# Kernel tuning notes

Measured on AMD Instinct MI355X. Metric: run time of the kernel, lower is better.

## Reference

```python
import jax, jax.numpy as jnp
import numpy as np

B, T, C, H, W, NC = 128, 32, 512, 8, 32, 6625
HH = C // 2  # per-direction LSTM hidden


def setup_inputs() -> dict:
    key = jax.random.key(0)
    ks = jax.random.split(key, 20)
    u = lambda k, shape, n: jax.random.uniform(k, shape, jnp.float32, -1.0 / np.sqrt(n), 1.0 / np.sqrt(n))
    return dict(
        feature=jax.random.normal(ks[0], (B, C, H, W), jnp.float32),
        attention_map=jax.random.uniform(ks[1], (B, T, H, W), jnp.float32) + 1e-3,
        text=jax.random.randint(ks[2], (B, T), 0, NC),
        text_length=jnp.full((B,), T, dtype=jnp.int32),
        char_embeddings=jax.random.normal(ks[3], (NC, C), jnp.float32),
        lstm_w_ih_f=u(ks[4], (4 * HH, C), HH),
        lstm_w_hh_f=u(ks[5], (4 * HH, HH), HH),
        lstm_b_ih_f=u(ks[6], (4 * HH,), HH),
        lstm_b_hh_f=u(ks[7], (4 * HH,), HH),
        lstm_w_ih_b=u(ks[8], (4 * HH, C), HH),
        lstm_w_hh_b=u(ks[9], (4 * HH, HH), HH),
        lstm_b_ih_b=u(ks[10], (4 * HH,), HH),
        lstm_b_hh_b=u(ks[11], (4 * HH,), HH),
        gru_w_ih=u(ks[12], (3 * C, 2 * C), C),
        gru_w_hh=u(ks[13], (3 * C, C), C),
        gru_b_ih=u(ks[14], (3 * C,), C),
        gru_b_hh=u(ks[15], (3 * C,), C),
        gen_w=u(ks[16], (NC, C), C),
        gen_b=u(ks[17], (NC,), C),
    )


def _lstm_dir(xs, w_ih, w_hh, b_ih, b_hh):
    # xs: [T, B, C] -> hs: [T, B, HH]; PyTorch gate order i, f, g, o
    b = xs.shape[1]
    hh = w_hh.shape[1]
    def step(carry, xt):
        h, c = carry
        g = xt @ w_ih.T + h @ w_hh.T + (b_ih + b_hh)
        i, f, gg, o = jnp.split(g, 4, axis=-1)
        c = jax.nn.sigmoid(f) * c + jax.nn.sigmoid(i) * jnp.tanh(gg)
        h = jax.nn.sigmoid(o) * jnp.tanh(c)
        return (h, c), h
    h0 = jnp.zeros((b, hh), xs.dtype)
    _, hs = jax.lax.scan(step, (h0, h0), xs)
    return hs


def reference(feature, attention_map, text, text_length, char_embeddings,
              lstm_w_ih_f, lstm_w_hh_f, lstm_b_ih_f, lstm_b_hh_f,
              lstm_w_ih_b, lstm_w_hh_b, lstm_b_ih_b, lstm_b_hh_b,
              gru_w_ih, gru_w_hh, gru_b_ih, gru_b_hh, gen_w, gen_b):
    b, c, h, w = feature.shape
    t = attention_map.shape[1]
    # normalize attention over spatial dims, attention-pool features: [T, B, C]
    att = attention_map / attention_map.sum(axis=(2, 3), keepdims=True)
    cseq = jnp.einsum('bchw,bthw->tbc', feature, att)
    # bidirectional LSTM (dropout is identity in eval mode)
    hs_f = _lstm_dir(cseq, lstm_w_ih_f, lstm_w_hh_f, lstm_b_ih_f, lstm_b_hh_f)
    hs_b = _lstm_dir(cseq[::-1], lstm_w_ih_b, lstm_w_hh_b, lstm_b_ih_b, lstm_b_hh_b)[::-1]
    cseq = jnp.concatenate([hs_f, hs_b], axis=-1)  # [T, B, C]
    # teacher-forced previous-char embeddings: step 0 uses index 0
    prev_idx = jnp.concatenate([jnp.zeros((b, 1), text.dtype), text[:, :-1]], axis=1)  # [B, T]
    prev_emb = jnp.transpose(char_embeddings[prev_idx], (1, 0, 2))  # [T, B, C]
    # GRUCell decode; PyTorch gate order r, z, n
    def gru_step(hid, inp):
        ct, pe = inp
        x = jnp.concatenate([ct, pe], axis=-1)  # [B, 2C]
        gi = x @ gru_w_ih.T + gru_b_ih
        gh = hid @ gru_w_hh.T + gru_b_hh
        ir, iz, inn = jnp.split(gi, 3, axis=-1)
        hr, hz, hn = jnp.split(gh, 3, axis=-1)
        r = jax.nn.sigmoid(ir + hr)
        z = jax.nn.sigmoid(iz + hz)
        n = jnp.tanh(inn + r * hn)
        hid = (1.0 - z) * n + z * hid
        return hid, hid
    h0 = jnp.zeros((b, c), cseq.dtype)
    _, gru_res = jax.lax.scan(gru_step, h0, (cseq, prev_emb))  # [T, B, C]
    logits = gru_res @ gen_w.T + gen_b  # [T, B, NC]
    # pack per text_length; lengths are all == T so this equals a reshape
    out_res = jnp.transpose(logits, (1, 0, 2)).reshape(b * t, -1)
    out_attentions = att.reshape(b * t, h, w)
    return (out_res, out_attentions)
```

## Files before the change

kernel.cpp:

```cpp
#include <hip/hip_runtime.h>
#include <math.h>

typedef __attribute__((ext_vector_type(8))) short sh8;
typedef __attribute__((ext_vector_type(4))) short sh4;
typedef __attribute__((ext_vector_type(4))) float f4;

__device__ inline short f2bf(float f) {
    union { float f; unsigned u; } v; v.f = f;
    unsigned u = v.u;
    return (short)((u + 0x7fffu + ((u >> 16) & 1u)) >> 16);
}
__device__ inline float sigm(float x) { return 1.f / (1.f + expf(-x)); }

__device__ inline sh8 frag8(const float* __restrict__ p) {
    f4 a = *(const f4*)p;
    f4 b = *(const f4*)(p + 4);
    sh8 r;
    r[0]=f2bf(a[0]); r[1]=f2bf(a[1]); r[2]=f2bf(a[2]); r[3]=f2bf(a[3]);
    r[4]=f2bf(b[0]); r[5]=f2bf(b[1]); r[6]=f2bf(b[2]); r[7]=f2bf(b[3]);
    return r;
}

__device__ inline sh8 cload_b128(const short* p) {
    sh8 r;
    asm volatile("global_load_dwordx4 %0, %1, off sc0 sc1" : "=v"(r) : "v"(p));
    return r;
}

__device__ inline void grp_signal(int* myflag, int epoch) {
    asm volatile("s_waitcnt vmcnt(0)" ::: "memory");
    __syncthreads();
    if (threadIdx.x == 0)
        __hip_atomic_store(myflag, epoch, __ATOMIC_RELAXED, __HIP_MEMORY_SCOPE_AGENT);
}
__device__ inline void grp_wait(const int* fbase, int nb, int epoch) {
    if (threadIdx.x < 64) {
        int lane = threadIdx.x;
        bool need = lane < nb;
        const int* fp = fbase + lane * 16;
        while (true) {
            int v = need ? __hip_atomic_load(fp, __ATOMIC_RELAXED, __HIP_MEMORY_SCOPE_AGENT)
                         : 0x7fffffff;
            if (__ballot(need && (v < epoch)) == 0ull) break;
            __builtin_amdgcn_s_sleep(1);
        }
    }
    __syncthreads();
}

__global__ void zero_ctr(int* c, int n) {
    int i = blockIdx.x * blockDim.x + threadIdx.x;
    if (i < n) c[i] = 0;
}

struct CvtPack { const float* s[7]; short* d[7]; int n4[7]; };
__global__ void cvt_bf16(CvtPack p) {
    int job = blockIdx.y;
    const f4* s = (const f4*)p.s[job];
    sh4* d = (sh4*)p.d[job];
    int n4 = p.n4[job];
    for (int i = blockIdx.x * blockDim.x + threadIdx.x; i < n4; i += gridDim.x * blockDim.x) {
        f4 v = s[i];
        sh4 o; o[0]=f2bf(v[0]); o[1]=f2bf(v[1]); o[2]=f2bf(v[2]); o[3]=f2bf(v[3]);
        d[i] = o;
    }
}

__global__ void bias_prep(const float* bihf, const float* bhhf,
                          const float* bihb, const float* bhhb, float* biasL) {
    int n = blockIdx.x * blockDim.x + threadIdx.x;
    biasL[n] = (n < 1024) ? bihf[n] + bhhf[n] : bihb[n - 1024] + bhhb[n - 1024];
}

__global__ void att_norm(const float* __restrict__ att, float* __restrict__ outA) {
    int row = blockIdx.x;
    int tid = threadIdx.x;
    const float* p = att + (size_t)row * 256;
    f4 v = *(const f4*)(p + tid * 4);
    float sum = v[0] + v[1] + v[2] + v[3];
    #pragma unroll
    for (int off = 32; off; off >>= 1) sum += __shfl_down(sum, off);
    float inv = 1.f / __shfl(sum, 0);
    f4 o; o[0]=v[0]*inv; o[1]=v[1]*inv; o[2]=v[2]*inv; o[3]=v[3]*inv;
    *(f4*)(outA + (size_t)row * 256 + tid * 4) = o;
}

__global__ __launch_bounds__(256)
void pool_gemm(const float* __restrict__ feature, const float* __restrict__ att,
               short* __restrict__ cseqb) {
    int bz = blockIdx.y;
    const float* A  = feature + (size_t)bz * 512 * 256;
    const float* Wt = att + (size_t)bz * 32 * 256;
    int wave = threadIdx.x >> 6, lane = threadIdx.x & 63, r = lane & 15, hh = lane >> 4;
    int m0 = blockIdx.x * 64 + wave * 16;
    f4 acc[2] = {};
    const float* ar = A  + (size_t)(m0 + r) * 256 + hh * 8;
    const float* w0 = Wt + (size_t)r * 256 + hh * 8;
    const float* w1 = Wt + (size_t)(16 + r) * 256 + hh * 8;
    for (int kk = 0; kk < 256; kk += 32) {
        sh8 af = frag8(ar + kk);
        acc[0] = __builtin_amdgcn_mfma_f32_16x16x32_bf16(af, frag8(w0 + kk), acc[0], 0, 0, 0);
        acc[1] = __builtin_amdgcn_mfma_f32_16x16x32_bf16(af, frag8(w1 + kk), acc[1], 0, 0, 0);
    }
    #pragma unroll
    for (int j = 0; j < 2; j++) {
        int t = j * 16 + r;
        #pragma unroll
        for (int reg = 0; reg < 4; reg++) {
            int c = m0 + hh * 4 + reg;
            cseqb[(size_t)t * 65536 + (size_t)bz * 512 + c] = f2bf(acc[j][reg]);
        }
    }
}

template<int MODE>
__global__ __launch_bounds__(256)
void gemm128(const short* __restrict__ A, const short* __restrict__ W,
             const float* __restrict__ bias1, const float* __restrict__ bias2,
             float* __restrict__ out, int M, int N, int K) {
    __shared__ short lds[2][2][4096];
    const int tid = threadIdx.x, wave = tid >> 6, lane = tid & 63;
    const int r = lane & 15, hh = lane >> 4;
    const int wm = wave >> 1, wn = wave & 1;
    const int m0 = blockIdx.x * 128, n0 = blockIdx.y * 128;

    const int c0 = tid, c1 = 256 + tid;
    const int r0 = c0 >> 2, r1 = c1 >> 2;
    const int s0 = ((c0 & 3) ^ ((r0 >> 1) & 3));
    const int s1 = ((c1 & 3) ^ ((r1 >> 1) & 3));
    const short* gA0 = A + (size_t)(m0 + r0) * K + s0 * 8;
    const short* gA1 = A + (size_t)(m0 + r1) * K + s1 * 8;
    int wr0 = n0 + r0; if (wr0 > N - 1) wr0 = N - 1;
    int wr1 = n0 + r1; if (wr1 > N - 1) wr1 = N - 1;
    const short* gW0 = W + (size_t)wr0 * K + s0 * 8;
    const short* gW1 = W + (size_t)wr1 * K + s1 * 8;
    const int lo0 = (wave * 64) * 8, lo1 = (256 + wave * 64) * 8;

    auto stage = [&](int buf, int kt) {
        int ko = kt * 32;
        __builtin_amdgcn_global_load_lds((const __attribute__((address_space(1))) void*)(gA0 + ko),
            (__attribute__((address_space(3))) void*)&lds[buf][0][lo0], 16, 0, 0);
        __builtin_amdgcn_global_load_lds((const __attribute__((address_space(1))) void*)(gA1 + ko),
            (__attribute__((address_space(3))) void*)&lds[buf][0][lo1], 16, 0, 0);
        __builtin_amdgcn_global_load_lds((const __attribute__((address_space(1))) void*)(gW0 + ko),
            (__attribute__((address_space(3))) void*)&lds[buf][1][lo0], 16, 0, 0);
        __builtin_amdgcn_global_load_lds((const __attribute__((address_space(1))) void*)(gW1 + ko),
            (__attribute__((address_space(3))) void*)&lds[buf][1][lo1], 16, 0, 0);
    };

    f4 acc[4][4] = {};
    const int NT = K / 32;
    int cur = 0;

    stage(0, 0);
    __syncthreads();
    for (int kt = 0; kt < NT; ++kt) {
        if (kt + 1 < NT) stage(cur ^ 1, kt + 1);
        const char* As = (const char*)&lds[cur][0][0];
        const char* Ws = (const char*)&lds[cur][1][0];
        sh8 a[4], b[4];
        #pragma unroll
        for (int i = 0; i < 4; i++) {
            int row = wm * 64 + i * 16 + r;
            a[i] = *(const sh8*)(As + row * 64 + ((hh ^ ((row >> 1) & 3)) * 16));
        }
        #pragma unroll
        for (int i = 0; i < 4; i++) {
            int row = wn * 64 + i * 16 + r;
            b[i] = *(const sh8*)(Ws + row * 64 + ((hh ^ ((row >> 1) & 3)) * 16));
        }
        #pragma unroll
        for (int i = 0; i < 4; i++)
            #pragma unroll
            for (int j = 0; j < 4; j++)
                acc[i][j] = __builtin_amdgcn_mfma_f32_16x16x32_bf16(a[i], b[j], acc[i][j], 0, 0, 0);
        __syncthreads();
        cur ^= 1;
    }

    #pragma unroll
    for (int j = 0; j < 4; j++) {
        int n = n0 + wn * 64 + j * 16 + r;
        if (n >= N) continue;
        float bs = (bias1 ? bias1[n] : 0.f) + (bias2 ? bias2[n] : 0.f);
        #pragma unroll
        for (int i = 0; i < 4; i++) {
            #pragma unroll
            for (int reg = 0; reg < 4; reg++) {
                int m = m0 + wm * 64 + i * 16 + hh * 4 + reg;
                size_t idx;
                if (MODE == 0) idx = (size_t)m * N + n;
                else           idx = ((size_t)(m & 127) * 32 + (m >> 7)) * (size_t)N + n;
                out[idx] = acc[i][j][reg] + bs;
            }
        }
    }
}

__global__ void emb_fill(const int* __restrict__ text, const float* __restrict__ emb,
                         short* __restrict__ xcatb) {
    int n = blockIdx.x;
    int t = n >> 7, b = n & 127;
    int idx = (t == 0) ? 0 : text[b * 32 + (t - 1)];
    const f4* src = (const f4*)(emb + (size_t)idx * 512);
    sh4* dst = (sh4*)(xcatb + (size_t)n * 1024 + 512);
    for (int j = threadIdx.x; j < 128; j += 64) {
        f4 v = src[j];
        sh4 o; o[0]=f2bf(v[0]); o[1]=f2bf(v[1]); o[2]=f2bf(v[2]); o[3]=f2bf(v[3]);
        dst[j] = o;
    }
}

__global__ __launch_bounds__(128)
void lstm_chain(const float* __restrict__ xfb,
                const short* __restrict__ whhf_b, const short* __restrict__ whhb_b,
                short* __restrict__ xcatb,
                int* __restrict__ flags) {
    __shared__ short wlds[64 * 256];
    const int blk = blockIdx.x;
    const int dir = blk >> 6;
    const int mg  = (blk >> 4) & 3;
    const int ug  = blk & 15;
    const int m0 = mg * 32, u0 = ug * 16;
    const short* whh = dir ? whhb_b : whhf_b;
    const int dcol = dir ? 256 : 0;

    int* grp_flags = flags + (dir * 4 + mg) * 16 * 16;
    int* my_flag   = grp_flags + ug * 16;

    const int tid = threadIdx.x, mt = tid >> 6, lane = tid & 63;
    const int r = lane & 15, hh = lane >> 4;
    unsigned* xcat32 = (unsigned*)xcatb;

    for (int i = 0; i < 16; i++) {
        int c = i * 128 + tid;
        int col = c >> 5, off = c & 31;
        int g = col >> 4, ul = col & 15;
        sh8 v = *(const sh8*)(whh + ((size_t)(g * 256 + u0 + ul)) * 256 + off * 8);
        *(sh8*)((char*)wlds + col * 512 + ((off * 16) ^ ((col & 7) << 4))) = v;
    }
    __syncthreads();

    const int arow_m = m0 + mt * 16 + r;
    const int u = u0 + r;
    const int mb = m0 + mt * 16 + hh * 4;
    float c_state[4] = {0.f, 0.f, 0.f, 0.f};

    float xv[4][4];
    {
        const int t0 = dir ? 31 : 0;
        #pragma unroll
        for (int g = 0; g < 4; g++)
            #pragma unroll
            for (int reg = 0; reg < 4; reg++)
                xv[g][reg] = xfb[((size_t)t0 * 128 + mb + reg) * 2048 + dir * 1024 + g * 256 + u];
    }

    for (int s = 0; s < 32; s++) {
        const int t = dir ? (31 - s) : s;
        f4 acc[4] = {};
        if (s > 0) {
            grp_wait(grp_flags, 16, s);
            const int tp = dir ? (t + 1) : (t - 1);
            const short* arow = xcatb + ((size_t)tp * 128 + arow_m) * 1024 + dcol + hh * 8;
            sh8 afr[8];
            #pragma unroll
            for (int kk = 0; kk < 8; kk++) afr[kk] = cload_b128(arow + kk * 32);
            asm volatile("s_waitcnt vmcnt(0)" ::: "memory");
            __builtin_amdgcn_sched_barrier(0);
            #pragma unroll
            for (int kk = 0; kk < 8; kk++) {
                #pragma unroll
                for (int g = 0; g < 4; g++) {
                    int colr = g * 16 + r;
                    sh8 bf = *(const sh8*)((const char*)wlds + colr * 512 +
                              (((kk * 64 + hh * 16)) ^ ((colr & 7) << 4)));
                    acc[g] = __builtin_amdgcn_mfma_f32_16x16x32_bf16(afr[kk], bf, acc[g], 0, 0, 0);
                }
            }
        }
        #pragma unroll
        for (int reg = 0; reg < 4; reg++) {
            int m = mb + reg;
            float gI = acc[0][reg] + xv[0][reg];
            float gF = acc[1][reg] + xv[1][reg];
            float gG = acc[2][reg] + xv[2][reg];
            float gO = acc[3][reg] + xv[3][reg];
            float cn = sigm(gF) * c_state[reg] + sigm(gI) * tanhf(gG);
            c_state[reg] = cn;
            float h = sigm(gO) * tanhf(cn);
            unsigned hb = (unsigned)(unsigned short)f2bf(h);
            unsigned pb = (unsigned)__shfl_xor((int)hb, 1, 64);
            if (!(r & 1))
                __hip_atomic_store(&xcat32[((size_t)t * 128 + m) * 512 + ((dcol + u) >> 1)],
                                   hb | (pb << 16), __ATOMIC_RELAXED, __HIP_MEMORY_SCOPE_AGENT);
        }
        if (s < 31) {
            grp_signal(my_flag, s + 1);
            const int tn = dir ? (t - 1) : (t + 1);
            #pragma unroll
            for (int g = 0; g < 4; g++)
                #pragma unroll
                for (int reg = 0; reg < 4; reg++)
                    xv[g][reg] = xfb[((size_t)tn * 128 + mb + reg) * 2048 + dir * 1024 + g * 256 + u];
        }
    }
}

__global__ __launch_bounds__(128)
void gru_chain(const float* __restrict__ gi,
               const short* __restrict__ gwhh_b, const float* __restrict__ bhh,
               short* __restrict__ gresb,
               int* __restrict__ flags) {
    __shared__ short wlds[48 * 512];
    const int blk = blockIdx.x;
    const int mg = blk >> 5, ug = blk & 31;
    const int m0 = mg * 32, u0 = ug * 16;

    int* grp_flags = flags + mg * 32 * 16;
    int* my_flag   = grp_flags + ug * 16;

    const int tid = threadIdx.x, mt = tid >> 6, lane = tid & 63;
    const int r = lane & 15, hh = lane >> 4;
    unsigned* gres32 = (unsigned*)gresb;

    for (int i = 0; i < 24; i++) {
        int c = i * 128 + tid;
        int col = c >> 6, off = c & 63;
        int g = col >> 4, ul = col & 15;
        sh8 v = *(const sh8*)(gwhh_b + ((size_t)(g * 512 + u0 + ul)) * 512 + off * 8);
        *(sh8*)((char*)wlds + col * 1024 + ((off * 16) ^ ((col & 7) << 4))) = v;
    }
    __syncthreads();

    const int arow_m = m0 + mt * 16 + r;
    const int u = u0 + r;
    const int mb = m0 + mt * 16 + hh * 4;
    const float bh_r = bhh[u], bh_z = bhh[512 + u], bh_n = bhh[1024 + u];
    float h_state[4] = {0.f, 0.f, 0.f, 0.f};

    float gv[3][4];
    #pragma unroll
    for (int g = 0; g < 3; g++)
        #pragma unroll
        for (int reg = 0; reg < 4; reg++)
            gv[g][reg] = gi[((size_t)(mb + reg)) * 1536 + g * 512 + u];

    for (int t = 0; t < 32; t++) {
        f4 acc[3] = {};
        if (t > 0) {
            grp_wait(grp_flags, 32, t);
            const short* arow = gresb + ((size_t)(t - 1) * 128 + arow_m) * 512 + hh * 8;
            sh8 afr[16];
            #pragma unroll
            for (int kk = 0; kk < 16; kk++) afr[kk] = cload_b128(arow + kk * 32);
            asm volatile("s_waitcnt vmcnt(0)" ::: "memory");
            __builtin_amdgcn_sched_barrier(0);
            #pragma unroll
            for (int kk = 0; kk < 16; kk++) {
                #pragma unroll
                for (int g = 0; g < 3; g++) {
                    int colr = g * 16 + r;
                    sh8 bf = *(const sh8*)((const char*)wlds + colr * 1024 +
                              (((kk * 64 + hh * 16)) ^ ((colr & 7) << 4)));
                    acc[g] = __builtin_amdgcn_mfma_f32_16x16x32_bf16(afr[kk], bf, acc[g], 0, 0, 0);
                }
            }
        }
        #pragma unroll
        for (int reg = 0; reg < 4; reg++) {
            int m = mb + reg;
            float rr = sigm(gv[0][reg] + acc[0][reg] + bh_r);
            float zz = sigm(gv[1][reg] + acc[1][reg] + bh_z);
            float nn = tanhf(gv[2][reg] + rr * (acc[2][reg] + bh_n));
            float h = (1.f - zz) * nn + zz * h_state[reg];
            h_state[reg] = h;
            unsigned hb = (unsigned)(unsigned short)f2bf(h);
            unsigned pb = (unsigned)__shfl_xor((int)hb, 1, 64);
            if (!(r & 1))
                __hip_atomic_store(&gres32[((size_t)t * 128 + m) * 256 + (u >> 1)],
                                   hb | (pb << 16), __ATOMIC_RELAXED, __HIP_MEMORY_SCOPE_AGENT);
        }
        if (t < 31) {
            grp_signal(my_flag, t + 1);
            #pragma unroll
            for (int g = 0; g < 3; g++)
                #pragma unroll
                for (int reg = 0; reg < 4; reg++)
                    gv[g][reg] = gi[((size_t)(t + 1) * 128 + mb + reg) * 1536 + g * 512 + u];
        }
    }
}

extern "C" void kernel_launch(void* const* d_in, const int* in_sizes, int n_in,
                              void* d_out, int out_size, void* d_ws, size_t ws_size,
                              hipStream_t stream) {
    const float* feature = (const float*)d_in[0];
    const float* attmap  = (const float*)d_in[1];
    const int*   text    = (const int*)d_in[2];
    const float* cemb    = (const float*)d_in[4];
    const float* wihf    = (const float*)d_in[5];
    const float* whhf    = (const float*)d_in[6];
    const float* bihf    = (const float*)d_in[7];
    const float* bhhf    = (const float*)d_in[8];
    const float* wihb    = (const float*)d_in[9];
    const float* whhb    = (const float*)d_in[10];
    const float* bihb    = (const float*)d_in[11];
    const float* bhhb    = (const float*)d_in[12];
    const float* gwih    = (const float*)d_in[13];
    const float* gwhh    = (const float*)d_in[14];
    const float* gbih    = (const float*)d_in[15];
    const float* gbhh    = (const float*)d_in[16];
    const float* genw    = (const float*)d_in[17];
    const float* genb    = (const float*)d_in[18];

    float* out    = (float*)d_out;
    float* outAtt = out + (size_t)4096 * 6625;

    float* xfb   = (float*)d_ws;
    float* gi    = xfb + 8388608;
    float* biasL = gi + 6291456;
    int*   flags = (int*)(biasL + 2048);
    short* cseqb  = (short*)(flags + 4096);
    short* xcatb  = cseqb + 2097152;
    short* gresb  = xcatb + 4194304;
    short* wih_b  = gresb + 2097152;
    short* whhf_b = wih_b + 1048576;
    short* whhb_b = whhf_b + 262144;
    short* gwih_b = whhb_b + 262144;
    short* gwhh_b = gwih_b + 1572864;
    short* genw_b = gwhh_b + 786432;

    zero_ctr<<<dim3(16), dim3(256), 0, stream>>>(flags, 4096);

    CvtPack p;
    p.s[0] = wihf; p.d[0] = wih_b;           p.n4[0] = 524288 / 4;
    p.s[1] = wihb; p.d[1] = wih_b + 524288;  p.n4[1] = 524288 / 4;
    p.s[2] = whhf; p.d[2] = whhf_b;          p.n4[2] = 262144 / 4;
    p.s[3] = whhb; p.d[3] = whhb_b;          p.n4[3] = 262144 / 4;
    p.s[4] = gwih; p.d[4] = gwih_b;          p.n4[4] = 1572864 / 4;
    p.s[5] = gwhh; p.d[5] = gwhh_b;          p.n4[5] = 786432 / 4;
    p.s[6] = genw; p.d[6] = genw_b;          p.n4[6] = 3392000 / 4;
    cvt_bf16<<<dim3(128, 7), dim3(256), 0, stream>>>(p);
    bias_prep<<<dim3(8), dim3(256), 0, stream>>>(bihf, bhhf, bihb, bhhb, biasL);

    att_norm<<<dim3(4096), dim3(64), 0, stream>>>(attmap, outAtt);
    pool_gemm<<<dim3(8, 128), dim3(256), 0, stream>>>(feature, outAtt, cseqb);

    gemm128<0><<<dim3(32, 16), dim3(256), 0, stream>>>(cseqb, wih_b, biasL, nullptr,
                                                       xfb, 4096, 2048, 512);
    emb_fill<<<dim3(4096), dim3(64), 0, stream>>>(text, cemb, xcatb);

    lstm_chain<<<dim3(128), dim3(128), 0, stream>>>(xfb, whhf_b, whhb_b, xcatb, flags);

    gemm128<0><<<dim3(32, 12), dim3(256), 0, stream>>>(xcatb, gwih_b, gbih, nullptr,
                                                       gi, 4096, 1536, 1024);

    gru_chain<<<dim3(128), dim3(128), 0, stream>>>(gi, gwhh_b, gbhh, gresb, flags + 2048);

    gemm128<1><<<dim3(32, 52), dim3(256), 0, stream>>>(gresb, genw_b, genb, nullptr,
                                                       out, 4096, 6625, 512);
}
```

Measured before the change: 432.4 us.

## Replace flag barriers with sentinel-polling on data; stage GEMM epilogue through LDS

The LSTM and GRU recurrent chains drop per-step flag signal/wait barriers. Consumers now poll the hidden-state buffers directly until no sentinel value remains, and producers remap any packed value that equals the sentinel so it is never written. This removes a syncthreads, a vmcnt drain and a flag round-trip from each step's critical path. Separately, the GEMM epilogue is staged through LDS so it can issue coalesced float4 stores, which matters most for the large transposed logits output. The risks are a full sentinel-fill pass over both buffers, repeated reloads while polling, and a tiny perturbation of bf16 values that collide with the sentinel.

New measurement: 453.8 us. +5.0%, slower.

```diff
diff --git a/kernel.cpp b/kernel.cpp
--- a/kernel.cpp
+++ b/kernel.cpp
@@ -4,6 +4,9 @@
 typedef __attribute__((ext_vector_type(8))) short sh8;
 typedef __attribute__((ext_vector_type(4))) short sh4;
 typedef __attribute__((ext_vector_type(4))) float f4;
+typedef __attribute__((ext_vector_type(4))) unsigned u4;
+
+#define SENT 0xFFFFFFFFu
 
 __device__ inline short f2bf(float f) {
     union { float f; unsigned u; } v; v.f = f;
@@ -11,6 +14,7 @@
     return (short)((u + 0x7fffu + ((u >> 16) & 1u)) >> 16);
 }
 __device__ inline float sigm(float x) { return 1.f / (1.f + expf(-x)); }
+__device__ inline sh8 as_sh8(u4 v) { union { u4 u; sh8 s; } c; c.u = v; return c.s; }
 
 __device__ inline sh8 frag8(const float* __restrict__ p) {
     f4 a = *(const f4*)p;
@@ -21,36 +25,22 @@
     return r;
 }
 
-__device__ inline sh8 cload_b128(const short* p) {
-    sh8 r;
+__device__ inline u4 cload_u4(const void* p) {
+    u4 r;
     asm volatile("global_load_dwordx4 %0, %1, off sc0 sc1" : "=v"(r) : "v"(p));
     return r;
 }
 
-__device__ inline void grp_signal(int* myflag, int epoch) {
-    asm volatile("s_waitcnt vmcnt(0)" ::: "memory");
-    __syncthreads();
-    if (threadIdx.x == 0)
-        __hip_atomic_store(myflag, epoch, __ATOMIC_RELAXED, __HIP_MEMORY_SCOPE_AGENT);
-}
-__device__ inline void grp_wait(const int* fbase, int nb, int epoch) {
-    if (threadIdx.x < 64) {
-        int lane = threadIdx.x;
-        bool need = lane < nb;
-        const int* fp = fbase + lane * 16;
-        while (true) {
-            int v = need ? __hip_atomic_load(fp, __ATOMIC_RELAXED, __HIP_MEMORY_SCOPE_AGENT)
-                         : 0x7fffffff;
-            if (__ballot(need && (v < epoch)) == 0ull) break;
-            __builtin_amdgcn_s_sleep(1);
-        }
-    }
-    __syncthreads();
-}
-
-__global__ void zero_ctr(int* c, int n) {
-    int i = blockIdx.x * blockDim.x + threadIdx.x;
-    if (i < n) c[i] = 0;
+__global__ void sent_fill(unsigned* __restrict__ xcat32, unsigned* __restrict__ gres32) {
+    unsigned i = blockIdx.x * blockDim.x + threadIdx.x;
+    u4 s = {SENT, SENT, SENT, SENT};
+    #pragma unroll
+    for (int k = 0; k < 2; k++) {
+        unsigned c = i + k * 131072;
+        unsigned row = c >> 6, off = c & 63;
+        *(u4*)(xcat32 + (size_t)row * 512 + off * 4) = s;
+        *(u4*)(gres32 + (size_t)c * 4) = s;
+    }
 }
 
 struct CvtPack { const float* s[7]; short* d[7]; int n4[7]; };
@@ -178,20 +168,44 @@
         cur ^= 1;
     }
 
+    float bsj[4];
     #pragma unroll
     for (int j = 0; j < 4; j++) {
         int n = n0 + wn * 64 + j * 16 + r;
-        if (n >= N) continue;
-        float bs = (bias1 ? bias1[n] : 0.f) + (bias2 ? bias2[n] : 0.f);
-        #pragma unroll
-        for (int i = 0; i < 4; i++) {
-            #pragma unroll
-            for (int reg = 0; reg < 4; reg++) {
-                int m = m0 + wm * 64 + i * 16 + hh * 4 + reg;
-                size_t idx;
-                if (MODE == 0) idx = (size_t)m * N + n;
-                else           idx = ((size_t)(m & 127) * 32 + (m >> 7)) * (size_t)N + n;
-                out[idx] = acc[i][j][reg] + bs;
+        int nc = n < N ? n : N - 1;
+        bsj[j] = (bias1 ? bias1[nc] : 0.f) + (bias2 ? bias2[nc] : 0.f);
+    }
+
+    float* fl = (float*)&lds[0][0][0];
+    #pragma unroll
+    for (int hhalf = 0; hhalf < 2; hhalf++) {
+        __syncthreads();
+        if (wm == hhalf) {
+            #pragma unroll
+            for (int i = 0; i < 4; i++)
+                #pragma unroll
+                for (int j = 0; j < 4; j++) {
+                    int col = wn * 64 + j * 16 + r;
+                    #pragma unroll
+                    for (int reg = 0; reg < 4; reg++)
+                        fl[(i * 16 + hh * 4 + reg) * 128 + col] = acc[i][j][reg] + bsj[j];
+                }
+        }
+        __syncthreads();
+        #pragma unroll
+        for (int it = 0; it < 8; it++) {
+            int c = it * 256 + tid;
+            int row = c >> 5, cf4 = c & 31;
+            int n = n0 + cf4 * 4;
+            int mrow = m0 + hhalf * 64 + row;
+            size_t orow = (MODE == 0) ? (size_t)mrow
+                                      : ((size_t)(mrow & 127) * 32 + (mrow >> 7));
+            if (n + 3 < N) {
+                *(f4*)&out[orow * N + n] = *(const f4*)&fl[row * 128 + cf4 * 4];
+            } else {
+                #pragma unroll
+                for (int d = 0; d < 4; d++)
+                    if (n + d < N) out[orow * N + n + d] = fl[row * 128 + cf4 * 4 + d];
             }
         }
     }
@@ -215,7 +229,7 @@
 void lstm_chain(const float* __restrict__ xfb,
                 const short* __restrict__ whhf_b, const short* __restrict__ whhb_b,
                 short* __restrict__ xcatb,
-                int* __restrict__ flags) {
+                int unused) {
     __shared__ short wlds[64 * 256];
     const int blk = blockIdx.x;
     const int dir = blk >> 6;
@@ -225,9 +239,6 @@
     const short* whh = dir ? whhb_b : whhf_b;
     const int dcol = dir ? 256 : 0;
 
-    int* grp_flags = flags + (dir * 4 + mg) * 16 * 16;
-    int* my_flag   = grp_flags + ug * 16;
-
     const int tid = threadIdx.x, mt = tid >> 6, lane = tid & 63;
     const int r = lane & 15, hh = lane >> 4;
     unsigned* xcat32 = (unsigned*)xcatb;
@@ -260,22 +271,31 @@
         const int t = dir ? (31 - s) : s;
         f4 acc[4] = {};
         if (s > 0) {
-            grp_wait(grp_flags, 16, s);
             const int tp = dir ? (t + 1) : (t - 1);
             const short* arow = xcatb + ((size_t)tp * 128 + arow_m) * 1024 + dcol + hh * 8;
-            sh8 afr[8];
-            #pragma unroll
-            for (int kk = 0; kk < 8; kk++) afr[kk] = cload_b128(arow + kk * 32);
-            asm volatile("s_waitcnt vmcnt(0)" ::: "memory");
-            __builtin_amdgcn_sched_barrier(0);
+            u4 afr[8];
+            while (true) {
+                #pragma unroll
+                for (int kk = 0; kk < 8; kk++) afr[kk] = cload_u4(arow + kk * 32);
+                asm volatile("s_waitcnt vmcnt(0)" ::: "memory");
+                __builtin_amdgcn_sched_barrier(0);
+                unsigned bad = 0;
+                #pragma unroll
+                for (int kk = 0; kk < 8; kk++)
+                    bad |= (afr[kk][0] == SENT) | (afr[kk][1] == SENT) |
+                           (afr[kk][2] == SENT) | (afr[kk][3] == SENT);
+                if (__ballot(bad != 0) == 0ull) break;
+                __builtin_amdgcn_s_sleep(1);
+            }
             #pragma unroll
             for (int kk = 0; kk < 8; kk++) {
+                sh8 af = as_sh8(afr[kk]);
                 #pragma unroll
                 for (int g = 0; g < 4; g++) {
                     int colr = g * 16 + r;
                     sh8 bf = *(const sh8*)((const char*)wlds + colr * 512 +
                               (((kk * 64 + hh * 16)) ^ ((colr & 7) << 4)));
-                    acc[g] = __builtin_amdgcn_mfma_f32_16x16x32_bf16(afr[kk], bf, acc[g], 0, 0, 0);
+                    acc[g] = __builtin_amdgcn_mfma_f32_16x16x32_bf16(af, bf, acc[g], 0, 0, 0);
                 }
             }
         }
@@ -291,12 +311,13 @@
             float h = sigm(gO) * tanhf(cn);
             unsigned hb = (unsigned)(unsigned short)f2bf(h);
             unsigned pb = (unsigned)__shfl_xor((int)hb, 1, 64);
+            unsigned pk = hb | (pb << 16);
+            pk = (pk == SENT) ? 0xFFFF7FFFu : pk;
             if (!(r & 1))
                 __hip_atomic_store(&xcat32[((size_t)t * 128 + m) * 512 + ((dcol + u) >> 1)],
-                                   hb | (pb << 16), __ATOMIC_RELAXED, __HIP_MEMORY_SCOPE_AGENT);
+                                   pk, __ATOMIC_RELAXED, __HIP_MEMORY_SCOPE_AGENT);
         }
         if (s < 31) {
-            grp_signal(my_flag, s + 1);
             const int tn = dir ? (t - 1) : (t + 1);
             #pragma unroll
             for (int g = 0; g < 4; g++)
@@ -311,14 +332,11 @@
 void gru_chain(const float* __restrict__ gi,
                const short* __restrict__ gwhh_b, const float* __restrict__ bhh,
                short* __restrict__ gresb,
-               int* __restrict__ flags) {
+               int unused) {
     __shared__ short wlds[48 * 512];
     const int blk = blockIdx.x;
     const int mg = blk >> 5, ug = blk & 31;
     const int m0 = mg * 32, u0 = ug * 16;
-
-    int* grp_flags = flags + mg * 32 * 16;
-    int* my_flag   = grp_flags + ug * 16;
 
     const int tid = threadIdx.x, mt = tid >> 6, lane = tid & 63;
     const int r = lane & 15, hh = lane >> 4;
@@ -349,21 +367,30 @@
     for (int t = 0; t < 32; t++) {
         f4 acc[3] = {};
         if (t > 0) {
-            grp_wait(grp_flags, 32, t);
             const short* arow = gresb + ((size_t)(t - 1) * 128 + arow_m) * 512 + hh * 8;
-            sh8 afr[16];
-            #pragma unroll
-            for (int kk = 0; kk < 16; kk++) afr[kk] = cload_b128(arow + kk * 32);
-            asm volatile("s_waitcnt vmcnt(0)" ::: "memory");
-            __builtin_amdgcn_sched_barrier(0);
+            u4 afr[16];
+            while (true) {
+                #pragma unroll
+                for (int kk = 0; kk < 16; kk++) afr[kk] = cload_u4(arow + kk * 32);
+                asm volatile("s_waitcnt vmcnt(0)" ::: "memory");
+                __builtin_amdgcn_sched_barrier(0);
+                unsigned bad = 0;
+                #pragma unroll
+                for (int kk = 0; kk < 16; kk++)
+                    bad |= (afr[kk][0] == SENT) | (afr[kk][1] == SENT) |
+                           (afr[kk][2] == SENT) | (afr[kk][3] == SENT);
+                if (__ballot(bad != 0) == 0ull) break;
+                __builtin_amdgcn_s_sleep(1);
+            }
             #pragma unroll
             for (int kk = 0; kk < 16; kk++) {
+                sh8 af = as_sh8(afr[kk]);
                 #pragma unroll
                 for (int g = 0; g < 3; g++) {
                     int colr = g * 16 + r;
                     sh8 bf = *(const sh8*)((const char*)wlds + colr * 1024 +
                               (((kk * 64 + hh * 16)) ^ ((colr & 7) << 4)));
-                    acc[g] = __builtin_amdgcn_mfma_f32_16x16x32_bf16(afr[kk], bf, acc[g], 0, 0, 0);
+                    acc[g] = __builtin_amdgcn_mfma_f32_16x16x32_bf16(af, bf, acc[g], 0, 0, 0);
                 }
             }
         }
@@ -377,12 +404,13 @@
             h_state[reg] = h;
             unsigned hb = (unsigned)(unsigned short)f2bf(h);
             unsigned pb = (unsigned)__shfl_xor((int)hb, 1, 64);
+            unsigned pk = hb | (pb << 16);
+            pk = (pk == SENT) ? 0xFFFF7FFFu : pk;
             if (!(r & 1))
                 __hip_atomic_store(&gres32[((size_t)t * 128 + m) * 256 + (u >> 1)],
-                                   hb | (pb << 16), __ATOMIC_RELAXED, __HIP_MEMORY_SCOPE_AGENT);
+                                   pk, __ATOMIC_RELAXED, __HIP_MEMORY_SCOPE_AGENT);
         }
         if (t < 31) {
-            grp_signal(my_flag, t + 1);
             #pragma unroll
             for (int g = 0; g < 3; g++)
                 #pragma unroll
@@ -420,8 +448,7 @@
     float* xfb   = (float*)d_ws;
     float* gi    = xfb + 8388608;
     float* biasL = gi + 6291456;
-    int*   flags = (int*)(biasL + 2048);
-    short* cseqb  = (short*)(flags + 4096);
+    short* cseqb  = (short*)(biasL + 2048);
     short* xcatb  = cseqb + 2097152;
     short* gresb  = xcatb + 4194304;
     short* wih_b  = gresb + 2097152;
@@ -431,7 +458,7 @@
     short* gwhh_b = gwih_b + 1572864;
     short* genw_b = gwhh_b + 786432;
 
-    zero_ctr<<<dim3(16), dim3(256), 0, stream>>>(flags, 4096);
+    sent_fill<<<dim3(512), dim3(256), 0, stream>>>((unsigned*)xcatb, (unsigned*)gresb);
 
     CvtPack p;
     p.s[0] = wihf; p.d[0] = wih_b;           p.n4[0] = 524288 / 4;
@@ -451,12 +478,12 @@
                                                        xfb, 4096, 2048, 512);
     emb_fill<<<dim3(4096), dim3(64), 0, stream>>>(text, cemb, xcatb);
 
-    lstm_chain<<<dim3(128), dim3(128), 0, stream>>>(xfb, whhf_b, whhb_b, xcatb, flags);
+    lstm_chain<<<dim3(128), dim3(128), 0, stream>>>(xfb, whhf_b, whhb_b, xcatb, 0);
 
     gemm128<0><<<dim3(32, 12), dim3(256), 0, stream>>>(xcatb, gwih_b, gbih, nullptr,
                                                        gi, 4096, 1536, 1024);
 
-    gru_chain<<<dim3(128), dim3(128), 0, stream>>>(gi, gwhh_b, gbhh, gresb, flags + 2048);
+    gru_chain<<<dim3(128), dim3(128), 0, stream>>>(gi, gwhh_b, gbhh, gresb, 0);
 
     gemm128<1><<<dim3(32, 52), dim3(256), 0, stream>>>(gresb, genw_b, genb, nullptr,
                                                        out, 4096, 6625, 512);
```

## Stage GEMM epilogue through LDS for vector stores; prefetch next-step gate inputs early

Applied to the files above, without the earlier changes.

The GEMM epilogue now writes accumulators (plus bias) into shared memory half a tile at a time, then stores them to global memory as coalesced float4 rows, with a scalar fallback at the N boundary. This replaces the previous scattered per-element stores, which were especially costly for the large vocabulary projection. In the LSTM and GRU recurrent chains, the next timestep's precomputed input gates are loaded with inline asm before the elementwise gate math, so their latency overlaps the activation work instead of following the signal. A sched_barrier is added in grp_signal to keep the waitcnt ordering intact. This costs extra LDS syncs and a few more live registers.

Measured after the change: 439.0 us. Within noise of the previous version (+1.5%).

```diff
diff --git a/kernel.cpp b/kernel.cpp
--- a/kernel.cpp
+++ b/kernel.cpp
@@ -4,6 +4,7 @@
 typedef __attribute__((ext_vector_type(8))) short sh8;
 typedef __attribute__((ext_vector_type(4))) short sh4;
 typedef __attribute__((ext_vector_type(4))) float f4;
+typedef __attribute__((ext_vector_type(4))) unsigned u4;
 
 __device__ inline short f2bf(float f) {
     union { float f; unsigned u; } v; v.f = f;
@@ -11,6 +12,7 @@
     return (short)((u + 0x7fffu + ((u >> 16) & 1u)) >> 16);
 }
 __device__ inline float sigm(float x) { return 1.f / (1.f + expf(-x)); }
+__device__ inline sh8 as_sh8(u4 v) { union { u4 u; sh8 s; } c; c.u = v; return c.s; }
 
 __device__ inline sh8 frag8(const float* __restrict__ p) {
     f4 a = *(const f4*)p;
@@ -21,14 +23,20 @@
     return r;
 }
 
-__device__ inline sh8 cload_b128(const short* p) {
-    sh8 r;
+__device__ inline u4 cload_u4(const void* p) {
+    u4 r;
     asm volatile("global_load_dwordx4 %0, %1, off sc0 sc1" : "=v"(r) : "v"(p));
     return r;
 }
+__device__ inline float ld_f32(const float* p) {
+    float r;
+    asm volatile("global_load_dword %0, %1, off" : "=v"(r) : "v"(p));
+    return r;
+}
 
 __device__ inline void grp_signal(int* myflag, int epoch) {
     asm volatile("s_waitcnt vmcnt(0)" ::: "memory");
+    __builtin_amdgcn_sched_barrier(0);
     __syncthreads();
     if (threadIdx.x == 0)
         __hip_atomic_store(myflag, epoch, __ATOMIC_RELAXED, __HIP_MEMORY_SCOPE_AGENT);
@@ -178,20 +186,44 @@
         cur ^= 1;
     }
 
+    float bsj[4];
     #pragma unroll
     for (int j = 0; j < 4; j++) {
         int n = n0 + wn * 64 + j * 16 + r;
-        if (n >= N) continue;
-        float bs = (bias1 ? bias1[n] : 0.f) + (bias2 ? bias2[n] : 0.f);
-        #pragma unroll
-        for (int i = 0; i < 4; i++) {
-            #pragma unroll
-            for (int reg = 0; reg < 4; reg++) {
-                int m = m0 + wm * 64 + i * 16 + hh * 4 + reg;
-                size_t idx;
-                if (MODE == 0) idx = (size_t)m * N + n;
-                else           idx = ((size_t)(m & 127) * 32 + (m >> 7)) * (size_t)N + n;
-                out[idx] = acc[i][j][reg] + bs;
+        int nc = n < N ? n : N - 1;
+        bsj[j] = (bias1 ? bias1[nc] : 0.f) + (bias2 ? bias2[nc] : 0.f);
+    }
+
+    float* fl = (float*)&lds[0][0][0];
+    #pragma unroll
+    for (int hhalf = 0; hhalf < 2; hhalf++) {
+        __syncthreads();
+        if (wm == hhalf) {
+            #pragma unroll
+            for (int i = 0; i < 4; i++)
+                #pragma unroll
+                for (int j = 0; j < 4; j++) {
+                    int col = wn * 64 + j * 16 + r;
+                    #pragma unroll
+                    for (int reg = 0; reg < 4; reg++)
+                        fl[(i * 16 + hh * 4 + reg) * 128 + col] = acc[i][j][reg] + bsj[j];
+                }
+        }
+        __syncthreads();
+        #pragma unroll
+        for (int it = 0; it < 8; it++) {
+            int c = it * 256 + tid;
+            int row = c >> 5, cf4 = c & 31;
+            int n = n0 + cf4 * 4;
+            int mrow = m0 + hhalf * 64 + row;
+            size_t orow = (MODE == 0) ? (size_t)mrow
+                                      : ((size_t)(mrow & 127) * 32 + (mrow >> 7));
+            if (n + 3 < N) {
+                *(f4*)&out[orow * N + n] = *(const f4*)&fl[row * 128 + cf4 * 4];
+            } else {
+                #pragma unroll
+                for (int d = 0; d < 4; d++)
+                    if (n + d < N) out[orow * N + n + d] = fl[row * 128 + cf4 * 4 + d];
             }
         }
     }
@@ -263,21 +295,32 @@
             grp_wait(grp_flags, 16, s);
             const int tp = dir ? (t + 1) : (t - 1);
             const short* arow = xcatb + ((size_t)tp * 128 + arow_m) * 1024 + dcol + hh * 8;
-            sh8 afr[8];
-            #pragma unroll
-            for (int kk = 0; kk < 8; kk++) afr[kk] = cload_b128(arow + kk * 32);
+            u4 afr[8];
+            #pragma unroll
+            for (int kk = 0; kk < 8; kk++) afr[kk] = cload_u4(arow + kk * 32);
             asm volatile("s_waitcnt vmcnt(0)" ::: "memory");
             __builtin_amdgcn_sched_barrier(0);
             #pragma unroll
             for (int kk = 0; kk < 8; kk++) {
+                sh8 af = as_sh8(afr[kk]);
                 #pragma unroll
                 for (int g = 0; g < 4; g++) {
                     int colr = g * 16 + r;
                     sh8 bf = *(const sh8*)((const char*)wlds + colr * 512 +
                               (((kk * 64 + hh * 16)) ^ ((colr & 7) << 4)));
-                    acc[g] = __builtin_amdgcn_mfma_f32_16x16x32_bf16(afr[kk], bf, acc[g], 0, 0, 0);
+                    acc[g] = __builtin_amdgcn_mfma_f32_16x16x32_bf16(af, bf, acc[g], 0, 0, 0);
                 }
             }
+        }
+        float xvn[4][4];
+        if (s < 31) {
+            const int tn = dir ? (t - 1) : (t + 1);
+            #pragma unroll
+            for (int g = 0; g < 4; g++)
+                #pragma unroll
+                for (int reg = 0; reg < 4; reg++)
+                    xvn[g][reg] = ld_f32(&xfb[((size_t)tn * 128 + mb + reg) * 2048 + dir * 1024 + g * 256 + u]);
+            asm volatile("" ::: "memory");
         }
         #pragma unroll
         for (int reg = 0; reg < 4; reg++) {
@@ -297,12 +340,11 @@
         }
         if (s < 31) {
             grp_signal(my_flag, s + 1);
-            const int tn = dir ? (t - 1) : (t + 1);
             #pragma unroll
             for (int g = 0; g < 4; g++)
                 #pragma unroll
                 for (int reg = 0; reg < 4; reg++)
-                    xv[g][reg] = xfb[((size_t)tn * 128 + mb + reg) * 2048 + dir * 1024 + g * 256 + u];
+                    xv[g][reg] = xvn[g][reg];
         }
     }
 }
@@ -351,21 +393,31 @@
         if (t > 0) {
             grp_wait(grp_flags, 32, t);
             const short* arow = gresb + ((size_t)(t - 1) * 128 + arow_m) * 512 + hh * 8;
-            sh8 afr[16];
-            #pragma unroll
-            for (int kk = 0; kk < 16; kk++) afr[kk] = cload_b128(arow + kk * 32);
+            u4 afr[16];
+            #pragma unroll
+            for (int kk = 0; kk < 16; kk++) afr[kk] = cload_u4(arow + kk * 32);
             asm volatile("s_waitcnt vmcnt(0)" ::: "memory");
             __builtin_amdgcn_sched_barrier(0);
             #pragma unroll
             for (int kk = 0; kk < 16; kk++) {
+                sh8 af = as_sh8(afr[kk]);
                 #pragma unroll
                 for (int g = 0; g < 3; g++) {
                     int colr = g * 16 + r;
                     sh8 bf = *(const sh8*)((const char*)wlds + colr * 1024 +
                               (((kk * 64 + hh * 16)) ^ ((colr & 7) << 4)));
-                    acc[g] = __builtin_amdgcn_mfma_f32_16x16x32_bf16(afr[kk], bf, acc[g], 0, 0, 0);
+                    acc[g] = __builtin_amdgcn_mfma_f32_16x16x32_bf16(af, bf, acc[g], 0, 0, 0);
                 }
             }
+        }
+        float gvn[3][4];
+        if (t < 31) {
+            #pragma unroll
+            for (int g = 0; g < 3; g++)
+                #pragma unroll
+                for (int reg = 0; reg < 4; reg++)
+                    gvn[g][reg] = ld_f32(&gi[((size_t)(t + 1) * 128 + mb + reg) * 1536 + g * 512 + u]);
+            asm volatile("" ::: "memory");
         }
         #pragma unroll
         for (int reg = 0; reg < 4; reg++) {
@@ -387,7 +439,7 @@
             for (int g = 0; g < 3; g++)
                 #pragma unroll
                 for (int reg = 0; reg < 4; reg++)
-                    gv[g][reg] = gi[((size_t)(t + 1) * 128 + mb + reg) * 1536 + g * 512 + u];
+                    gv[g][reg] = gvn[g][reg];
         }
     }
 }
```
